# Kernel optimization log

Measured on AMD Instinct MI355X. Metric: run time of the kernel, lower is better.

## Reference

```python
import jax, jax.numpy as jnp
import numpy as np

NUM_CLASSES = 80
D_IMG = 2048
D_WORD = 300
D_MID = 1024
B = 8
CONV = 14


def setup_inputs() -> dict:
    key = jax.random.key(0)
    ks = jax.random.split(key, 6)
    s = lambda k, shape, sc: jax.random.normal(k, shape, dtype=jnp.float32) * sc
    return {
        "batch_size": B,
        "img_feature_map": jax.random.normal(ks[0], (B, D_IMG, CONV, CONV), dtype=jnp.float32),
        "word_features": jax.random.normal(ks[1], (NUM_CLASSES, D_WORD), dtype=jnp.float32),
        "W1": s(ks[2], (D_MID, D_IMG), 0.02),
        "W2": s(ks[3], (D_MID, D_WORD), 0.02),
        "W3": s(ks[4], (D_MID, D_MID), 0.02),
        "b3": jnp.zeros((D_MID,), jnp.float32),
        "Wa": s(ks[5], (1, D_MID), 0.02),
        "ba": jnp.zeros((1,), jnp.float32),
    }


def reference(batch_size, img_feature_map, word_features, W1, W2, W3, b3, Wa, ba):
    # img_feature_map: [B, D_img, H, W] -> [B, H, W, D_img] (matches torch double transpose)
    Bn, D, H, W = img_feature_map.shape
    fmap = jnp.transpose(img_feature_map, (0, 2, 3, 1))                 # [B,H,W,D]
    f_wh = jnp.einsum('bhwd,md->bhwm', fmap, W1)                        # fc_1: [B,H,W,M]
    f_wd = word_features @ W2.T                                         # fc_2: [C,M]
    # broadcast multiply (no explicit repeat) + tanh
    t = jnp.tanh(f_wh[:, :, :, None, :] * f_wd)                         # [B,H,W,C,M]
    lb = jnp.einsum('bhwcm,nm->bhwcn', t, W3) + b3                      # fc_3: [B,H,W,C,M]
    coef = jnp.einsum('bhwcm,m->bhwc', lb, Wa[0]) + ba[0]               # fc_a: [B,H,W,C]
    # softmax over spatial positions per (batch, class)
    C = coef.shape[-1]
    coef = jax.nn.softmax(coef.reshape(Bn, H * W, C), axis=1).reshape(Bn, H, W, C)
    # softmax-weighted spatial pooling -> [B, C, D]
    return jnp.einsum('bhwc,bhwd->bcd', coef, fmap)
```

## Files before the change

### kernel.cpp

```cpp
#include <hip/hip_runtime.h>
#include <hip/hip_bf16.h>
#include <stdint.h>

#define NB 8
#define DIMG 2048
#define HWN 196
#define PN 1568
#define PPAD 1600
#define DMID 1024
#define NC 80
#define DWORD 300
#define PART 16

typedef short bf16x8 __attribute__((ext_vector_type(8)));
typedef float f32x4 __attribute__((ext_vector_type(4)));

__device__ __forceinline__ unsigned short f2bf(float x) {
  union { float f; unsigned u; } c; c.f = x;
  unsigned r = c.u + 0x7FFFu + ((c.u >> 16) & 1u);
  return (unsigned short)(r >> 16);
}

__global__ void k_tc(const float* __restrict__ img, unsigned short* __restrict__ fmapH,
                     const float* __restrict__ W1, unsigned short* __restrict__ W1h) {
  __shared__ float tile[32][33];
  int bx = blockIdx.x;
  int tx = threadIdx.x, ty = threadIdx.y;
  if (bx < 3584) {
    int d0 = (bx & 63) * 32;
    int rem = bx >> 6;
    int h0 = (rem % 7) * 32, b = rem / 7;
    const float* src = img + (size_t)b * DIMG * HWN;
#pragma unroll
    for (int i = 0; i < 32; i += 8) {
      int hw = h0 + tx;
      tile[ty + i][tx] = (hw < HWN) ? src[(size_t)(d0 + ty + i) * HWN + hw] : 0.f;
    }
    __syncthreads();
#pragma unroll
    for (int i = 0; i < 32; i += 8) {
      int hw = h0 + ty + i;
      if (hw < HWN)
        fmapH[(size_t)(b * HWN + hw) * DIMG + d0 + tx] = f2bf(tile[tx][ty + i]);
    }
  } else {
    int tid = ty * 32 + tx;
    int i = ((bx - 3584) * 256 + tid) * 4;
    f32x4 v = *(const f32x4*)(W1 + i);
    ushort4 s;
    s.x = f2bf(v[0]); s.y = f2bf(v[1]); s.z = f2bf(v[2]); s.w = f2bf(v[3]);
    *(ushort4*)(W1h + i) = s;
  }
}

__global__ __launch_bounds__(256) void k_fwdweff(const float* __restrict__ word,
                                                 const float* __restrict__ W2,
                                                 float* __restrict__ fwd,
                                                 const float* __restrict__ Wa,
                                                 const float* __restrict__ W3,
                                                 float* __restrict__ partial) {
  __shared__ __align__(16) float w2s[64 * DWORD];
  __shared__ __align__(16) float wds[16 * DWORD];
  int bx = blockIdx.x, t = threadIdx.x;
  if (bx < 80) {
    int m0 = (bx & 15) * 64, c0 = (bx >> 4) * 16;
    const float SC = 2.8853900817779268f;
    for (int u = t; u < 64 * 75; u += 256) {
      int r = u / 75, q = u - r * 75;
      *(f32x4*)&w2s[r * DWORD + q * 4] =
          *(const f32x4*)(W2 + (size_t)(m0 + r) * DWORD + q * 4);
    }
    for (int u = t; u < 16 * 75; u += 256) {
      int r = u / 75, q = u - r * 75;
      f32x4 v = *(const f32x4*)(word + (size_t)(c0 + r) * DWORD + q * 4);
      *(f32x4*)&wds[r * DWORD + q * 4] = v * SC;
    }
    __syncthreads();
    int ci = t >> 4, mi = t & 15;
    f32x4 a0 = {0.f, 0.f, 0.f, 0.f}, a1 = a0, a2 = a0, a3 = a0;
    const float* wr = &wds[ci * DWORD];
    for (int q = 0; q < 75; ++q) {
      f32x4 wv = *(const f32x4*)&wr[q * 4];
      f32x4 b0 = *(const f32x4*)&w2s[(mi)*DWORD + q * 4];
      f32x4 b1 = *(const f32x4*)&w2s[(mi + 16) * DWORD + q * 4];
      f32x4 b2 = *(const f32x4*)&w2s[(mi + 32) * DWORD + q * 4];
      f32x4 b3 = *(const f32x4*)&w2s[(mi + 48) * DWORD + q * 4];
#pragma unroll
      for (int u = 0; u < 4; ++u) {
        a0[u] = fmaf(wv[u], b0[u], a0[u]);
        a1[u] = fmaf(wv[u], b1[u], a1[u]);
        a2[u] = fmaf(wv[u], b2[u], a2[u]);
        a3[u] = fmaf(wv[u], b3[u], a3[u]);
      }
    }
    float* dst = fwd + (size_t)(c0 + ci) * DMID + m0 + mi;
    dst[0]  = a0[0] + a0[1] + a0[2] + a0[3];
    dst[16] = a1[0] + a1[1] + a1[2] + a1[3];
    dst[32] = a2[0] + a2[1] + a2[2] + a2[3];
    dst[48] = a3[0] + a3[1] + a3[2] + a3[3];
  } else {
    int idx = bx - 80;
    int m = (idx & 3) * 256 + t;
    int n0 = (idx >> 2) * 64;
    float acc = 0.f;
    for (int n = n0; n < n0 + 64; ++n) acc = fmaf(Wa[n], W3[(size_t)n * DMID + m], acc);
    partial[(size_t)(idx >> 2) * DMID + m] = acc;
  }
}

#define GLDS(g, l) \
  __builtin_amdgcn_global_load_lds((const __attribute__((address_space(1))) void*)(g), \
                                   (__attribute__((address_space(3))) void*)(l), 16, 0, 0)

__global__ __launch_bounds__(256) void k_fused(const unsigned short* __restrict__ A,
                                               const unsigned short* __restrict__ Bw,
                                               const float* __restrict__ fwd,
                                               const float* __restrict__ partial,
                                               float* __restrict__ coefp) {
  __shared__ __align__(16) char smem[49152];
  unsigned short* As = (unsigned short*)smem;
  unsigned short* Bs = As + 3 * 4096;
  float* Xl = (float*)smem;
  float* bl = Xl + 64 * 68;
  float* wl = bl + 80 * 68;
  int p0 = blockIdx.x * 64, mz = blockIdx.y;
  int n0 = mz * 64;
  int t = threadIdx.x;
  int w = t >> 6, l = t & 63;
  int wr = w >> 1, wc = w & 1;
  f32x4 zero = {0.f, 0.f, 0.f, 0.f};
  f32x4 acc00 = zero, acc01 = zero, acc10 = zero, acc11 = zero;

  int r0 = t >> 3, cch = t & 7;
  int r1 = r0 + 32;
  const unsigned short* ga0 = A + (size_t)(p0 + r0) * 2048 + ((cch ^ (r0 & 7)) << 3);
  const unsigned short* ga1 = A + (size_t)(p0 + r1) * 2048 + ((cch ^ (r1 & 7)) << 3);
  const unsigned short* gb0 = Bw + (size_t)(n0 + r0) * 2048 + ((cch ^ (r0 & 7)) << 3);
  const unsigned short* gb1 = Bw + (size_t)(n0 + r1) * 2048 + ((cch ^ (r1 & 7)) << 3);

  int ra = wr * 32 + (l & 15);
  int rb = wc * 32 + (l & 15);
  int cc = l >> 4;
  int a_k0 = ra * 64 + (((cc) ^ (ra & 7)) << 3);
  int a_k1 = ra * 64 + (((cc + 4) ^ (ra & 7)) << 3);
  int b_k0 = rb * 64 + (((cc) ^ (rb & 7)) << 3);
  int b_k1 = rb * 64 + (((cc + 4) ^ (rb & 7)) << 3);

#define STAGE(bi, kk) do { \
    GLDS(ga0 + (kk), As + (bi) * 4096 + t * 8); \
    GLDS(ga1 + (kk), As + (bi) * 4096 + t * 8 + 2048); \
    GLDS(gb0 + (kk), Bs + (bi) * 4096 + t * 8); \
    GLDS(gb1 + (kk), Bs + (bi) * 4096 + t * 8 + 2048); \
  } while (0)

#define COMPUTE(bi) do { \
    const unsigned short* ap = As + (bi) * 4096; \
    const unsigned short* bp = Bs + (bi) * 4096; \
    bf16x8 A0 = *(const bf16x8*)(ap + a_k0); \
    bf16x8 A1 = *(const bf16x8*)(ap + a_k0 + 1024); \
    bf16x8 B0 = *(const bf16x8*)(bp + b_k0); \
    bf16x8 B1 = *(const bf16x8*)(bp + b_k0 + 1024); \
    acc00 = __builtin_amdgcn_mfma_f32_16x16x32_bf16(A0, B0, acc00, 0, 0, 0); \
    acc01 = __builtin_amdgcn_mfma_f32_16x16x32_bf16(A0, B1, acc01, 0, 0, 0); \
    acc10 = __builtin_amdgcn_mfma_f32_16x16x32_bf16(A1, B0, acc10, 0, 0, 0); \
    acc11 = __builtin_amdgcn_mfma_f32_16x16x32_bf16(A1, B1, acc11, 0, 0, 0); \
    bf16x8 A2 = *(const bf16x8*)(ap + a_k1); \
    bf16x8 A3 = *(const bf16x8*)(ap + a_k1 + 1024); \
    bf16x8 B2 = *(const bf16x8*)(bp + b_k1); \
    bf16x8 B3 = *(const bf16x8*)(bp + b_k1 + 1024); \
    acc00 = __builtin_amdgcn_mfma_f32_16x16x32_bf16(A2, B2, acc00, 0, 0, 0); \
    acc01 = __builtin_amdgcn_mfma_f32_16x16x32_bf16(A2, B3, acc01, 0, 0, 0); \
    acc10 = __builtin_amdgcn_mfma_f32_16x16x32_bf16(A3, B2, acc10, 0, 0, 0); \
    acc11 = __builtin_amdgcn_mfma_f32_16x16x32_bf16(A3, B3, acc11, 0, 0, 0); \
  } while (0)

  STAGE(0, 0);
  STAGE(1, 64);
  asm volatile("s_waitcnt vmcnt(4)" ::: "memory");
  __builtin_amdgcn_s_barrier();
  __builtin_amdgcn_sched_barrier(0);
  for (int kt = 0; kt < 32; ++kt) {
    int cur = kt % 3;
    if (kt < 30) STAGE((kt + 2) % 3, (kt + 2) * 64);
    COMPUTE(cur);
    if (kt < 30) {
      asm volatile("s_waitcnt vmcnt(4)" ::: "memory");
      __builtin_amdgcn_s_barrier();
      __builtin_amdgcn_sched_barrier(0);
    } else if (kt == 30) {
      asm volatile("s_waitcnt vmcnt(0)" ::: "memory");
      __builtin_amdgcn_s_barrier();
      __builtin_amdgcn_sched_barrier(0);
    }
  }
  __syncthreads();

  {
    int cr = (l >> 4) << 2, ccn = l & 15;
#pragma unroll
    for (int q = 0; q < 4; ++q) {
      Xl[(wr * 32 + cr + q) * 68 + wc * 32 + ccn]      = acc00[q];
      Xl[(wr * 32 + cr + q) * 68 + wc * 32 + 16 + ccn] = acc01[q];
      Xl[(wr * 32 + 16 + cr + q) * 68 + wc * 32 + ccn]      = acc10[q];
      Xl[(wr * 32 + 16 + cr + q) * 68 + wc * 32 + 16 + ccn] = acc11[q];
    }
#pragma unroll
    for (int i = 0; i < 5; ++i) {
      int idx = t + 256 * i;
      int r = idx >> 4, c4 = (idx & 15) << 2;
      *(f32x4*)&bl[r * 68 + c4] = *(const f32x4*)(fwd + (size_t)r * DMID + n0 + c4);
    }
    if (t < 64) {
      float v = 0.f;
#pragma unroll
      for (int s = 0; s < 16; ++s) v += partial[(size_t)s * DMID + n0 + t];
      wl[t] = -2.f * v;
    }
  }
  __syncthreads();

  int pi = t >> 4, ci = t & 15;
  float acc[4][5];
#pragma unroll
  for (int j = 0; j < 4; ++j)
#pragma unroll
    for (int k = 0; k < 5; ++k) acc[j][k] = 0.f;

#pragma unroll 1
  for (int mm = 0; mm < 64; mm += 4) {
    f32x4 wv = *(const f32x4*)&wl[mm];
    f32x4 av0 = *(const f32x4*)&Xl[(pi)*68 + mm];
    f32x4 av1 = *(const f32x4*)&Xl[(pi + 16) * 68 + mm];
    f32x4 av2 = *(const f32x4*)&Xl[(pi + 32) * 68 + mm];
    f32x4 av3 = *(const f32x4*)&Xl[(pi + 48) * 68 + mm];
#pragma unroll
    for (int k = 0; k < 5; ++k) {
      f32x4 bv = *(const f32x4*)&bl[(k * 16 + ci) * 68 + mm];
#pragma unroll
      for (int u = 0; u < 4; ++u) {
        float wgt = wv[u], b = bv[u];
        float e0 = __builtin_amdgcn_exp2f(av0[u] * b);
        float e1 = __builtin_amdgcn_exp2f(av1[u] * b);
        float e2 = __builtin_amdgcn_exp2f(av2[u] * b);
        float e3 = __builtin_amdgcn_exp2f(av3[u] * b);
        acc[0][k] = fmaf(wgt, __builtin_amdgcn_rcpf(1.f + e0), acc[0][k]);
        acc[1][k] = fmaf(wgt, __builtin_amdgcn_rcpf(1.f + e1), acc[1][k]);
        acc[2][k] = fmaf(wgt, __builtin_amdgcn_rcpf(1.f + e2), acc[2][k]);
        acc[3][k] = fmaf(wgt, __builtin_amdgcn_rcpf(1.f + e3), acc[3][k]);
      }
    }
  }
  float* cp = coefp + (size_t)mz * (PN * NC);
#pragma unroll
  for (int j = 0; j < 4; ++j) {
    int p = p0 + pi + 16 * j;
    if (p < PN) {
#pragma unroll
      for (int k = 0; k < 5; ++k)
        cp[(size_t)p * NC + k * 16 + ci] = acc[j][k];
    }
  }
#undef STAGE
#undef COMPUTE
}

__global__ __launch_bounds__(256) void k_pool(const float* __restrict__ coefp,
                                              const float* __restrict__ img,
                                              float* __restrict__ out) {
  __shared__ __align__(16) float wt[HWN][16];
  __shared__ float red[16][16];
  __shared__ float mxs[16], inv[16];
  int dc = blockIdx.x * 256, cg = blockIdx.y * 16, b = blockIdx.z;
  int t = threadIdx.x;
  for (int i = t; i < HWN * 4; i += 256) {
    int hw = i >> 2, j4 = (i & 3) << 2;
    size_t o = (size_t)(b * HWN + hw) * NC + cg + j4;
    f32x4 s = {0.f, 0.f, 0.f, 0.f};
#pragma unroll
    for (int z = 0; z < PART; ++z) s += *(const f32x4*)&coefp[o + (size_t)z * (PN * NC)];
    *(f32x4*)&wt[hw][j4] = s;
  }
  __syncthreads();
  int j = t & 15, g = t >> 4;
  float pm = -1e30f;
  for (int hw = g; hw < HWN; hw += 16) pm = fmaxf(pm, wt[hw][j]);
  red[g][j] = pm;
  __syncthreads();
  if (t < 16) {
    float m = red[0][t];
#pragma unroll
    for (int g2 = 1; g2 < 16; ++g2) m = fmaxf(m, red[g2][t]);
    mxs[t] = m;
  }
  __syncthreads();
  float mj = mxs[j], ps = 0.f;
  for (int hw = g; hw < HWN; hw += 16) {
    float e = __builtin_amdgcn_exp2f((wt[hw][j] - mj) * 1.4426950408889634f);
    wt[hw][j] = e;
    ps += e;
  }
  red[g][j] = ps;
  __syncthreads();
  if (t < 16) {
    float s = 0.f;
#pragma unroll
    for (int g2 = 0; g2 < 16; ++g2) s += red[g2][t];
    inv[t] = 1.f / s;
  }
  __syncthreads();
  float acc[16];
#pragma unroll
  for (int q = 0; q < 16; ++q) acc[q] = 0.f;
  const float* fpd = img + ((size_t)b * DIMG + dc + t) * HWN;
  for (int hw = 0; hw < HWN; ++hw) {
    float v = fpd[hw];
#pragma unroll
    for (int q = 0; q < 16; ++q) acc[q] = fmaf(wt[hw][q], v, acc[q]);
  }
#pragma unroll
  for (int q = 0; q < 16; ++q)
    out[((size_t)b * NC + cg + q) * DIMG + dc + t] = acc[q] * inv[q];
}

extern "C" void kernel_launch(void* const* d_in, const int* in_sizes, int n_in,
                              void* d_out, int out_size, void* d_ws, size_t ws_size,
                              hipStream_t stream) {
  const float* img  = (const float*)d_in[1];
  const float* word = (const float*)d_in[2];
  const float* W1   = (const float*)d_in[3];
  const float* W2   = (const float*)d_in[4];
  const float* W3   = (const float*)d_in[5];
  const float* Wa   = (const float*)d_in[7];
  float* out = (float*)d_out;
  char* ws = (char*)d_ws;

  unsigned short* fmapH   = (unsigned short*)(ws + 0);
  unsigned short* W1h     = (unsigned short*)(ws + 6553600);
  float*          fwd     = (float*)(ws + 10747904);
  float*          partial = (float*)(ws + 11141120);
  float*          coefp   = (float*)(ws + 11206656);

  hipLaunchKernelGGL(k_tc, dim3(5632), dim3(32, 8), 0, stream, img, fmapH, W1, W1h);
  hipLaunchKernelGGL(k_fwdweff, dim3(144), dim3(256), 0, stream,
                     word, W2, fwd, Wa, W3, partial);
  hipLaunchKernelGGL(k_fused, dim3(25, 16), dim3(256), 0, stream,
                     fmapH, W1h, fwd, partial, coefp);
  hipLaunchKernelGGL(k_pool, dim3(8, 5, 8), dim3(256), 0, stream, coefp, img, out);
  (void)in_sizes; (void)n_in; (void)out_size; (void)ws_size;
}
```

Before: 110.5 us.

## Halve fused GEMM M-tile to 32 rows and double grid, add MFMA priority

```diff
diff --git a/kernel.cpp b/kernel.cpp
--- a/kernel.cpp
+++ b/kernel.cpp
@@ -117,29 +117,27 @@
                                                const float* __restrict__ fwd,
                                                const float* __restrict__ partial,
                                                float* __restrict__ coefp) {
-  __shared__ __align__(16) char smem[49152];
+  __shared__ __align__(16) char smem[36864];
   unsigned short* As = (unsigned short*)smem;
-  unsigned short* Bs = As + 3 * 4096;
+  unsigned short* Bs = As + 3 * 2048;
   float* Xl = (float*)smem;
-  float* bl = Xl + 64 * 68;
+  float* bl = Xl + 32 * 68;
   float* wl = bl + 80 * 68;
-  int p0 = blockIdx.x * 64, mz = blockIdx.y;
+  int p0 = blockIdx.x * 32, mz = blockIdx.y;
   int n0 = mz * 64;
   int t = threadIdx.x;
   int w = t >> 6, l = t & 63;
-  int wr = w >> 1, wc = w & 1;
   f32x4 zero = {0.f, 0.f, 0.f, 0.f};
-  f32x4 acc00 = zero, acc01 = zero, acc10 = zero, acc11 = zero;
+  f32x4 acc0 = zero, acc1 = zero;
 
   int r0 = t >> 3, cch = t & 7;
   int r1 = r0 + 32;
   const unsigned short* ga0 = A + (size_t)(p0 + r0) * 2048 + ((cch ^ (r0 & 7)) << 3);
-  const unsigned short* ga1 = A + (size_t)(p0 + r1) * 2048 + ((cch ^ (r1 & 7)) << 3);
   const unsigned short* gb0 = Bw + (size_t)(n0 + r0) * 2048 + ((cch ^ (r0 & 7)) << 3);
   const unsigned short* gb1 = Bw + (size_t)(n0 + r1) * 2048 + ((cch ^ (r1 & 7)) << 3);
 
-  int ra = wr * 32 + (l & 15);
-  int rb = wc * 32 + (l & 15);
+  int ra = l & 15;
+  int rb = w * 16 + (l & 15);
   int cc = l >> 4;
   int a_k0 = ra * 64 + (((cc) ^ (ra & 7)) << 3);
   int a_k1 = ra * 64 + (((cc + 4) ^ (ra & 7)) << 3);
@@ -147,36 +145,33 @@
   int b_k1 = rb * 64 + (((cc + 4) ^ (rb & 7)) << 3);
 
 #define STAGE(bi, kk) do { \
-    GLDS(ga0 + (kk), As + (bi) * 4096 + t * 8); \
-    GLDS(ga1 + (kk), As + (bi) * 4096 + t * 8 + 2048); \
+    GLDS(ga0 + (kk), As + (bi) * 2048 + t * 8); \
     GLDS(gb0 + (kk), Bs + (bi) * 4096 + t * 8); \
     GLDS(gb1 + (kk), Bs + (bi) * 4096 + t * 8 + 2048); \
   } while (0)
 
 #define COMPUTE(bi) do { \
-    const unsigned short* ap = As + (bi) * 4096; \
+    const unsigned short* ap = As + (bi) * 2048; \
     const unsigned short* bp = Bs + (bi) * 4096; \
     bf16x8 A0 = *(const bf16x8*)(ap + a_k0); \
     bf16x8 A1 = *(const bf16x8*)(ap + a_k0 + 1024); \
     bf16x8 B0 = *(const bf16x8*)(bp + b_k0); \
-    bf16x8 B1 = *(const bf16x8*)(bp + b_k0 + 1024); \
-    acc00 = __builtin_amdgcn_mfma_f32_16x16x32_bf16(A0, B0, acc00, 0, 0, 0); \
-    acc01 = __builtin_amdgcn_mfma_f32_16x16x32_bf16(A0, B1, acc01, 0, 0, 0); \
-    acc10 = __builtin_amdgcn_mfma_f32_16x16x32_bf16(A1, B0, acc10, 0, 0, 0); \
-    acc11 = __builtin_amdgcn_mfma_f32_16x16x32_bf16(A1, B1, acc11, 0, 0, 0); \
+    __builtin_amdgcn_s_setprio(1); \
+    acc0 = __builtin_amdgcn_mfma_f32_16x16x32_bf16(A0, B0, acc0, 0, 0, 0); \
+    acc1 = __builtin_amdgcn_mfma_f32_16x16x32_bf16(A1, B0, acc1, 0, 0, 0); \
+    __builtin_amdgcn_s_setprio(0); \
     bf16x8 A2 = *(const bf16x8*)(ap + a_k1); \
     bf16x8 A3 = *(const bf16x8*)(ap + a_k1 + 1024); \
-    bf16x8 B2 = *(const bf16x8*)(bp + b_k1); \
-    bf16x8 B3 = *(const bf16x8*)(bp + b_k1 + 1024); \
-    acc00 = __builtin_amdgcn_mfma_f32_16x16x32_bf16(A2, B2, acc00, 0, 0, 0); \
-    acc01 = __builtin_amdgcn_mfma_f32_16x16x32_bf16(A2, B3, acc01, 0, 0, 0); \
-    acc10 = __builtin_amdgcn_mfma_f32_16x16x32_bf16(A3, B2, acc10, 0, 0, 0); \
-    acc11 = __builtin_amdgcn_mfma_f32_16x16x32_bf16(A3, B3, acc11, 0, 0, 0); \
+    bf16x8 B1 = *(const bf16x8*)(bp + b_k1); \
+    __builtin_amdgcn_s_setprio(1); \
+    acc0 = __builtin_amdgcn_mfma_f32_16x16x32_bf16(A2, B1, acc0, 0, 0, 0); \
+    acc1 = __builtin_amdgcn_mfma_f32_16x16x32_bf16(A3, B1, acc1, 0, 0, 0); \
+    __builtin_amdgcn_s_setprio(0); \
   } while (0)
 
   STAGE(0, 0);
   STAGE(1, 64);
-  asm volatile("s_waitcnt vmcnt(4)" ::: "memory");
+  asm volatile("s_waitcnt vmcnt(3)" ::: "memory");
   __builtin_amdgcn_s_barrier();
   __builtin_amdgcn_sched_barrier(0);
   for (int kt = 0; kt < 32; ++kt) {
@@ -184,7 +179,7 @@
     if (kt < 30) STAGE((kt + 2) % 3, (kt + 2) * 64);
     COMPUTE(cur);
     if (kt < 30) {
-      asm volatile("s_waitcnt vmcnt(4)" ::: "memory");
+      asm volatile("s_waitcnt vmcnt(3)" ::: "memory");
       __builtin_amdgcn_s_barrier();
       __builtin_amdgcn_sched_barrier(0);
     } else if (kt == 30) {
@@ -196,13 +191,11 @@
   __syncthreads();
 
   {
-    int cr = (l >> 4) << 2, ccn = l & 15;
+    int xr = (l >> 4) << 2, xc = w * 16 + (l & 15);
 #pragma unroll
     for (int q = 0; q < 4; ++q) {
-      Xl[(wr * 32 + cr + q) * 68 + wc * 32 + ccn]      = acc00[q];
-      Xl[(wr * 32 + cr + q) * 68 + wc * 32 + 16 + ccn] = acc01[q];
-      Xl[(wr * 32 + 16 + cr + q) * 68 + wc * 32 + ccn]      = acc10[q];
-      Xl[(wr * 32 + 16 + cr + q) * 68 + wc * 32 + 16 + ccn] = acc11[q];
+      Xl[(xr + q) * 68 + xc]        = acc0[q];
+      Xl[(xr + q + 16) * 68 + xc]   = acc1[q];
     }
 #pragma unroll
     for (int i = 0; i < 5; ++i) {
@@ -220,9 +213,9 @@
   __syncthreads();
 
   int pi = t >> 4, ci = t & 15;
-  float acc[4][5];
-#pragma unroll
-  for (int j = 0; j < 4; ++j)
+  float acc[2][5];
+#pragma unroll
+  for (int j = 0; j < 2; ++j)
 #pragma unroll
     for (int k = 0; k < 5; ++k) acc[j][k] = 0.f;
 
@@ -231,8 +224,6 @@
     f32x4 wv = *(const f32x4*)&wl[mm];
     f32x4 av0 = *(const f32x4*)&Xl[(pi)*68 + mm];
     f32x4 av1 = *(const f32x4*)&Xl[(pi + 16) * 68 + mm];
-    f32x4 av2 = *(const f32x4*)&Xl[(pi + 32) * 68 + mm];
-    f32x4 av3 = *(const f32x4*)&Xl[(pi + 48) * 68 + mm];
 #pragma unroll
     for (int k = 0; k < 5; ++k) {
       f32x4 bv = *(const f32x4*)&bl[(k * 16 + ci) * 68 + mm];
@@ -241,18 +232,14 @@
         float wgt = wv[u], b = bv[u];
         float e0 = __builtin_amdgcn_exp2f(av0[u] * b);
         float e1 = __builtin_amdgcn_exp2f(av1[u] * b);
-        float e2 = __builtin_amdgcn_exp2f(av2[u] * b);
-        float e3 = __builtin_amdgcn_exp2f(av3[u] * b);
         acc[0][k] = fmaf(wgt, __builtin_amdgcn_rcpf(1.f + e0), acc[0][k]);
         acc[1][k] = fmaf(wgt, __builtin_amdgcn_rcpf(1.f + e1), acc[1][k]);
-        acc[2][k] = fmaf(wgt, __builtin_amdgcn_rcpf(1.f + e2), acc[2][k]);
-        acc[3][k] = fmaf(wgt, __builtin_amdgcn_rcpf(1.f + e3), acc[3][k]);
       }
     }
   }
   float* cp = coefp + (size_t)mz * (PN * NC);
 #pragma unroll
-  for (int j = 0; j < 4; ++j) {
+  for (int j = 0; j < 2; ++j) {
     int p = p0 + pi + 16 * j;
     if (p < PN) {
 #pragma unroll
@@ -343,7 +330,7 @@
   hipLaunchKernelGGL(k_tc, dim3(5632), dim3(32, 8), 0, stream, img, fmapH, W1, W1h);
   hipLaunchKernelGGL(k_fwdweff, dim3(144), dim3(256), 0, stream,
                      word, W2, fwd, Wa, W3, partial);
-  hipLaunchKernelGGL(k_fused, dim3(25, 16), dim3(256), 0, stream,
+  hipLaunchKernelGGL(k_fused, dim3(50, 16), dim3(256), 0, stream,
                      fmapH, W1h, fwd, partial, coefp);
   hipLaunchKernelGGL(k_pool, dim3(8, 5, 8), dim3(256), 0, stream, coefp, img, out);
   (void)in_sizes; (void)n_in; (void)out_size; (void)ws_size;
```

New measurement: 111.0 us. About the same (+0.4%).
